# Kernel tuning notes

Hardware: AMD Instinct MI355X
Metric: run time of the kernel (lower is better)

The kernel has to match this reference:

```python
import jax, jax.numpy as jnp
import numpy as np

RESOLUTIONS = [33, 65, 129, 257, 513]
BAL = 0.5
K_CONFLICT = 3  # fixed unrolled conflict-resolution passes per level


def _up2(x):
    """Exact 2x-1 bilinear upsample with align_corners=True. [H,W]->[2H-1,2W-1]."""
    H, W = x.shape
    y = jnp.zeros((2 * H - 1, W), x.dtype)
    y = y.at[::2].set(x).at[1::2].set(0.5 * (x[:-1] + x[1:]))
    z = jnp.zeros((2 * H - 1, 2 * W - 1), x.dtype)
    z = z.at[:, ::2].set(y).at[:, 1::2].set(0.5 * (y[:, :-1] + y[:, 1:]))
    return z


def _any3x3(mask):
    """3x3 'smooth conv > 0' == any neighbor true. bool [H,W] -> bool [H,W]."""
    x = mask.astype(jnp.float32)[None, None]
    k = jnp.ones((1, 1, 3, 3), jnp.float32)
    y = jax.lax.conv_general_dilated(x, k, (1, 1), ((1, 1), (1, 1)))
    return y[0, 0] > 0


def setup_inputs() -> dict:
    key = jax.random.key(0)
    ks = jax.random.split(key, 4)
    d = 128
    return {
        "W1": jax.random.normal(ks[0], (2, d), jnp.float32) * 1.0,
        "b1": jnp.zeros((d,), jnp.float32),
        "W2": jax.random.normal(ks[1], (d, d), jnp.float32) / np.sqrt(d),
        "b2": jnp.zeros((d,), jnp.float32),
        "W3": jax.random.normal(ks[2], (d, 1), jnp.float32) * (2.0 / np.sqrt(d)),
        "b3": jnp.zeros((1,), jnp.float32),
        "b_min": jnp.zeros((2,), jnp.float32),
        "b_max": jnp.ones((2,), jnp.float32),
    }


def reference(W1, b1, W2, b2, W3, b3, b_min, b_max):
    def eval_grid(H, W):
        # align_corners=True: grid coords / (res-1) in [0,1], identical at every level
        u = jnp.linspace(0.0, 1.0, W, dtype=jnp.float32)
        v = jnp.linspace(0.0, 1.0, H, dtype=jnp.float32)
        X, Y = jnp.meshgrid(u, v)          # [H,W] each
        pts = jnp.stack([X, Y], -1).reshape(-1, 2)
        pts = b_min + pts * (b_max - b_min)
        h = jnp.tanh(pts @ W1 + b1)
        h = jnp.tanh(h @ W2 + b2)
        return jax.nn.sigmoid(h @ W3 + b3).reshape(H, W)

    Rf = RESOLUTIONS[-1]
    R0 = RESOLUTIONS[0]
    occ = eval_grid(R0, R0)                       # level-0 full evaluation
    calc = jnp.zeros((Rf, Rf), bool)
    s0 = (Rf - 1) // (R0 - 1)
    calc = calc.at[::s0, ::s0].set(True)

    for R in RESOLUTIONS[1:]:
        s = (Rf - 1) // (R - 1)
        occ_i = _up2(occ)                          # bilinear interp, align_corners=True
        valid = _up2((occ > BAL).astype(occ.dtype))
        boundary = (valid > 0) & (valid < 1)       # crossing band
        boundary = _any3x3(boundary)               # smooth_conv3x3 > 0
        calc_lvl = calc[::s, ::s]
        boundary = boundary & ~calc_lvl            # exclude already-evaluated points
        q = eval_grid(R, R)                        # query_func on level grid (masked use)
        conflicts = boundary & ((occ_i - BAL) * (q - BAL) < 0)
        occ = jnp.where(boundary, q, occ_i)        # scatter query values at boundary
        calc_lvl = calc_lvl | boundary
        # conflict resolution: re-evaluate 8-neighborhood of conflicting points
        for _ in range(K_CONFLICT):
            cand = _any3x3(conflicts) & ~calc_lvl
            conflicts = cand & ((occ - BAL) * (q - BAL) < 0)
            occ = jnp.where(cand, q, occ)
            calc_lvl = calc_lvl | cand
        calc = calc.at[::s, ::s].set(calc_lvl)

    return occ[None, None]                         # [1, 1, Rf, Rf]
```

## Files before the change

kernel.cpp:

```cpp
#include <hip/hip_runtime.h>

typedef unsigned char u8;
typedef float f32x4 __attribute__((ext_vector_type(4)));
typedef _Float16 f16x8 __attribute__((ext_vector_type(8)));

#define DIM 128
#define TM  128

__device__ __forceinline__ float fast_tanh(float x) {
    float e = __builtin_amdgcn_exp2f(x * 2.885390081777927f);
    return 1.0f - 2.0f * __builtin_amdgcn_rcpf(e + 1.0f);
}
__device__ __forceinline__ float fast_sigmoid(float x) {
    float e = __builtin_amdgcn_exp2f(x * -1.4426950408889634f);
    return __builtin_amdgcn_rcpf(1.0f + e);
}

template<int NT>
__device__ __forceinline__ void stage_w2(const float* __restrict__ W2,
                                         _Float16* sW2T, int tid) {
    #pragma unroll
    for (int s = 0; s < 2048 / NT; ++s) {
        int chunk = s * NT + tid;
        int n = chunk & 127, ko = chunk >> 7;
        f16x8 v;
        #pragma unroll
        for (int qq = 0; qq < 8; ++qq)
            v[qq] = (_Float16)W2[(ko * 8 + qq) * DIM + n];
        int slot = ko ^ (n & 15);
        *(f16x8*)&sW2T[n * DIM + slot * 8] = v;
    }
}

__device__ __forceinline__ void mlp_wave(
    const float xs[2], const float ys[2], const _Float16* sW2T,
    const float* __restrict__ W1, const float* __restrict__ b1,
    const float* __restrict__ b2, const float* __restrict__ W3,
    int lg, int l15, float rs[2][4])
{
    f32x4 acc[2][8];
    #pragma unroll
    for (int nf = 0; nf < 8; ++nf) {
        float b2v = b2[nf * 16 + l15];
        acc[0][nf] = (f32x4)(b2v);
        acc[1][nf] = (f32x4)(b2v);
    }
    #pragma unroll
    for (int kf = 0; kf < 4; ++kf) {
        const int kbase = kf * 32 + lg * 8;
        f16x8 bh[8];
        #pragma unroll
        for (int nf = 0; nf < 8; ++nf) {
            int cc = nf * 16 + l15;
            int slot = (kf * 4 + lg) ^ l15;
            bh[nf] = *(const f16x8*)&sW2T[cc * DIM + slot * 8];
        }
        f32x4 wxa = *(const f32x4*)&W1[kbase];
        f32x4 wxb = *(const f32x4*)&W1[kbase + 4];
        f32x4 wya = *(const f32x4*)&W1[DIM + kbase];
        f32x4 wyb = *(const f32x4*)&W1[DIM + kbase + 4];
        f32x4 b1a = *(const f32x4*)&b1[kbase];
        f32x4 b1b = *(const f32x4*)&b1[kbase + 4];
        f16x8 ah[2];
        #pragma unroll
        for (int mf = 0; mf < 2; ++mf) {
            float x = xs[mf], y = ys[mf];
            #pragma unroll
            for (int qq = 0; qq < 4; ++qq)
                ah[mf][qq] = (_Float16)fast_tanh(fmaf(x, wxa[qq], fmaf(y, wya[qq], b1a[qq])));
            #pragma unroll
            for (int qq = 0; qq < 4; ++qq)
                ah[mf][4 + qq] = (_Float16)fast_tanh(fmaf(x, wxb[qq], fmaf(y, wyb[qq], b1b[qq])));
        }
        #pragma unroll
        for (int nf = 0; nf < 8; ++nf)
            #pragma unroll
            for (int mf = 0; mf < 2; ++mf)
                acc[mf][nf] = __builtin_amdgcn_mfma_f32_16x16x32_f16(ah[mf], bh[nf], acc[mf][nf], 0, 0, 0);
    }
    #pragma unroll
    for (int mf = 0; mf < 2; ++mf)
        #pragma unroll
        for (int rg = 0; rg < 4; ++rg) rs[mf][rg] = 0.0f;
    #pragma unroll
    for (int nf = 0; nf < 8; ++nf) {
        float w3v = W3[nf * 16 + l15];
        #pragma unroll
        for (int mf = 0; mf < 2; ++mf)
            #pragma unroll
            for (int rg = 0; rg < 4; ++rg)
                rs[mf][rg] += fast_tanh(acc[mf][nf][rg]) * w3v;
    }
    #pragma unroll
    for (int mf = 0; mf < 2; ++mf)
        #pragma unroll
        for (int rg = 0; rg < 4; ++rg) {
            float v = rs[mf][rg];
            v += __shfl_xor(v, 1);
            v += __shfl_xor(v, 2);
            v += __shfl_xor(v, 4);
            v += __shfl_xor(v, 8);
            rs[mf][rg] = v;
        }
}

__global__ __launch_bounds__(256, 4) void eval_grid(
    const float* __restrict__ W1, const float* __restrict__ b1,
    const float* __restrict__ W2, const float* __restrict__ b2,
    const float* __restrict__ W3, const float* __restrict__ b3,
    const float* __restrict__ bmin, const float* __restrict__ bmax,
    float* __restrict__ out, int R)
{
    __shared__ __align__(16) _Float16 sW2T[DIM * DIM];
    const int N = R * R;
    const int tid = threadIdx.x;
    const int m0 = blockIdx.x * TM;
    stage_w2<256>(W2, sW2T, tid);

    const int w = tid >> 6, lane = tid & 63;
    const int l15 = lane & 15, lg = lane >> 4;

    const float inv = 1.0f / (float)(R - 1);
    const float bx0 = bmin[0], by0 = bmin[1];
    const float sx = bmax[0] - bx0, sy = bmax[1] - by0;
    float xs[2], ys[2];
    #pragma unroll
    for (int mf = 0; mf < 2; ++mf) {
        int pi = m0 + w * 32 + mf * 16 + l15;
        int pg = (pi < N) ? pi : N - 1;
        int gi = pg / R, gj = pg - gi * R;
        xs[mf] = bx0 + (float)gj * inv * sx;
        ys[mf] = by0 + (float)gi * inv * sy;
    }
    __syncthreads();

    float rs[2][4];
    mlp_wave(xs, ys, sW2T, W1, b1, b2, W3, lg, l15, rs);
    if (l15 == 0) {
        float b3v = b3[0];
        #pragma unroll
        for (int mf = 0; mf < 2; ++mf)
            #pragma unroll
            for (int rg = 0; rg < 4; ++rg) {
                int po = m0 + w * 32 + mf * 16 + lg * 4 + rg;
                if (po < N) out[po] = fast_sigmoid(rs[mf][rg] + b3v);
            }
    }
}

__global__ __launch_bounds__(512, 4) void eval_fine(
    const float* __restrict__ W1, const float* __restrict__ b1,
    const float* __restrict__ W2, const float* __restrict__ b2,
    const float* __restrict__ W3, const float* __restrict__ b3,
    const float* __restrict__ bmin, const float* __restrict__ bmax,
    const float* __restrict__ occ3, float* __restrict__ q4)
{
    __shared__ __align__(16) _Float16 sW2T[DIM * DIM];
    const int bi = blockIdx.x / 33, bj = blockIdx.x - bi * 33;
    const int ti0 = bi * 16, tj0 = bj * 16;
    const int tid = threadIdx.x;

    bool need = false;
    for (int s = tid; s < 576; s += 512) {
        int li = s / 24, lj = s - li * 24;
        int fi = ti0 - 4 + li, fj = tj0 - 4 + lj;
        if (fi >= 0 && fi < 513 && fj >= 0 && fj < 513) {
            int oi = fi & 1, oj = fj & 1;
            if (oi | oj) {
                int ip = fi >> 1, jp = fj >> 1;
                bool m0 = occ3[ip * 257 + jp] > 0.5f;
                bool b;
                if (oi && !oj)      b = m0 != (occ3[(ip + 1) * 257 + jp] > 0.5f);
                else if (!oi && oj) b = m0 != (occ3[ip * 257 + jp + 1] > 0.5f);
                else {
                    bool m1 = occ3[(ip + 1) * 257 + jp] > 0.5f;
                    bool m2 = occ3[ip * 257 + jp + 1] > 0.5f;
                    bool m3 = occ3[(ip + 1) * 257 + jp + 1] > 0.5f;
                    b = (m0 | m1 | m2 | m3) && !(m0 & m1 & m2 & m3);
                }
                need |= b;
            }
        }
    }
    if (!__syncthreads_or(need ? 1 : 0)) return;

    stage_w2<512>(W2, sW2T, tid);
    __syncthreads();

    const int w = tid >> 6, lane = tid & 63;
    const int l15 = lane & 15, lg = lane >> 4;
    const float inv = 1.0f / 512.0f;
    const float bx0 = bmin[0], by0 = bmin[1];
    const float sx = bmax[0] - bx0, sy = bmax[1] - by0;

    float xs[2], ys[2];
    #pragma unroll
    for (int mf = 0; mf < 2; ++mf) {
        int p = w * 32 + mf * 16 + l15;
        int gi = ti0 + (p >> 4), gj = tj0 + (p & 15);
        if (gi > 512) gi = 512;
        if (gj > 512) gj = 512;
        xs[mf] = bx0 + (float)gj * inv * sx;
        ys[mf] = by0 + (float)gi * inv * sy;
    }
    float rs[2][4];
    mlp_wave(xs, ys, sW2T, W1, b1, b2, W3, lg, l15, rs);
    if (l15 == 0) {
        float b3v = b3[0];
        #pragma unroll
        for (int mf = 0; mf < 2; ++mf)
            #pragma unroll
            for (int rg = 0; rg < 4; ++rg) {
                int p = w * 32 + mf * 16 + lg * 4 + rg;
                int gi = ti0 + (p >> 4), gj = tj0 + (p & 15);
                if (gi < 513 && gj < 513)
                    q4[gi * 513 + gj] = fast_sigmoid(rs[mf][rg] + b3v);
            }
    }
}

#define HWF 24
#define NTF 576
template<bool FIRST>
__device__ __forceinline__ void run_level(
    int c, int li, int lj, int oi0, int oj0, int R,
    const float* __restrict__ qbuf, int qpitch, int qs,
    const float* __restrict__ q257, int pOi, int pOj,
    const float* sOccP, const u8* sCalP,
    u8* sRaw, u8* sCfA, u8* sCfB,
    float& occR, bool& calR)
{
    const float BAL = 0.5f;
    const int fi = oi0 + li, fj = oj0 + lj;
    const bool inG = (fi >= 0 && fi < R && fj >= 0 && fj < R);
    float occ = 0.5f, qv = 0.5f;
    u8 rw = 0; bool cal = false;
    if (inG) qv = qbuf[(fi * qs) * qpitch + fj * qs];
    if (inG) {
        int ip = fi >> 1, jp = fj >> 1;
        int oi = fi & 1, oj = fj & 1;
        float tl = FIRST ? q257[(ip * 8) * 257 + jp * 8]
                         : sOccP[(ip - pOi) * HWF + (jp - pOj)];
        bool b;
        if (!oi && !oj) { occ = tl; b = false; }
        else if (oi && !oj) {
            float bl = FIRST ? q257[((ip + 1) * 8) * 257 + jp * 8]
                             : sOccP[(ip + 1 - pOi) * HWF + (jp - pOj)];
            occ = 0.5f * (tl + bl);
            b = (tl > BAL) != (bl > BAL);
        } else if (!oi && oj) {
            float tr = FIRST ? q257[(ip * 8) * 257 + (jp + 1) * 8]
                             : sOccP[(ip - pOi) * HWF + (jp + 1 - pOj)];
            occ = 0.5f * (tl + tr);
            b = (tl > BAL) != (tr > BAL);
        } else {
            float bl = FIRST ? q257[((ip + 1) * 8) * 257 + jp * 8]
                             : sOccP[(ip + 1 - pOi) * HWF + (jp - pOj)];
            float tr = FIRST ? q257[(ip * 8) * 257 + (jp + 1) * 8]
                             : sOccP[(ip - pOi) * HWF + (jp + 1 - pOj)];
            float br = FIRST ? q257[((ip + 1) * 8) * 257 + (jp + 1) * 8]
                             : sOccP[(ip + 1 - pOi) * HWF + (jp + 1 - pOj)];
            occ = 0.5f * (0.5f * (tl + bl) + 0.5f * (tr + br));
            bool m0 = tl > BAL, m1 = bl > BAL, m2 = tr > BAL, m3 = br > BAL;
            b = (m0 | m1 | m2 | m3) && !(m0 & m1 & m2 & m3);
        }
        rw = b ? 1 : 0;
        if (((fi | fj) & 1) == 0)
            cal = FIRST ? true : (sCalP[(ip - pOi) * HWF + (jp - pOj)] != 0);
    }
    sRaw[c] = rw; sCfA[c] = 0; sCfB[c] = 0;

    if (__syncthreads_or(rw)) {
        u8 cf = 0;
        if (li >= 1 && li < HWF - 1 && lj >= 1 && lj < HWF - 1 && inG) {
            bool b = false;
            #pragma unroll
            for (int di = -1; di <= 1; ++di)
                #pragma unroll
                for (int dj = -1; dj <= 1; ++dj)
                    if (sRaw[(li + di) * HWF + (lj + dj)]) b = true;
            b = b && !cal;
            cf = (b && (occ - BAL) * (qv - BAL) < 0.0f) ? 1 : 0;
            if (b) { occ = qv; cal = true; }
            sCfA[c] = cf;
        }
        int haveCf = __syncthreads_or((int)cf);

        #pragma unroll
        for (int it = 0; it < 3; ++it) {
            if (!haveCf) break;
            const u8* cin = (it & 1) ? sCfB : sCfA;
            u8* cout      = (it & 1) ? sCfA : sCfB;
            int lo = 2 + it, hi = HWF - 2 - it;
            u8 nc = 0;
            if (li >= lo && li < hi && lj >= lo && lj < hi && inG) {
                bool any = false;
                #pragma unroll
                for (int di = -1; di <= 1; ++di)
                    #pragma unroll
                    for (int dj = -1; dj <= 1; ++dj)
                        if (cin[(li + di) * HWF + (lj + dj)]) any = true;
                bool cand = any && !cal;
                nc = (cand && (occ - BAL) * (qv - BAL) < 0.0f) ? 1 : 0;
                if (cand) { occ = qv; cal = true; }
                cout[c] = nc;
            }
            haveCf = __syncthreads_or((int)nc);
        }
    }
    occR = occ; calR = cal;
}

__global__ __launch_bounds__(NTF) void levels123_fused(
    const float* __restrict__ q257,
    float* __restrict__ occ257, u8* __restrict__ cal257)
{
    __shared__ float sOcc[NTF];
    __shared__ u8 sCal[NTF], sRaw[NTF], sCfA[NTF], sCfB[NTF];
    const int bi = blockIdx.x / 17, bj = blockIdx.x - bi * 17;
    const int c = threadIdx.x;
    const int li = c / HWF, lj = c - li * HWF;
    float occ; bool cal;

    run_level<true>(c, li, lj, 4 * bi - 7, 4 * bj - 7, 65,
                    q257, 257, 4, q257, 0, 0,
                    sOcc, sCal, sRaw, sCfA, sCfB, occ, cal);
    sOcc[c] = occ; sCal[c] = cal ? 1 : 0;
    __syncthreads();
    run_level<false>(c, li, lj, 8 * bi - 6, 8 * bj - 6, 129,
                     q257, 257, 2, q257, 4 * bi - 7, 4 * bj - 7,
                     sOcc, sCal, sRaw, sCfA, sCfB, occ, cal);
    sOcc[c] = occ; sCal[c] = cal ? 1 : 0;
    __syncthreads();
    run_level<false>(c, li, lj, 16 * bi - 4, 16 * bj - 4, 257,
                     q257, 257, 1, q257, 8 * bi - 6, 8 * bj - 6,
                     sOcc, sCal, sRaw, sCfA, sCfB, occ, cal);

    const int fi = 16 * bi - 4 + li, fj = 16 * bj - 4 + lj;
    if (li >= 4 && li < 20 && lj >= 4 && lj < 20 && fi < 257 && fj < 257) {
        occ257[fi * 257 + fj] = occ;
        cal257[fi * 257 + fj] = cal ? 1 : 0;
    }
}

__global__ __launch_bounds__(NTF) void level4_kernel(
    const float* __restrict__ occP, const u8* __restrict__ calcP,
    const float* __restrict__ q4, float* __restrict__ out)
{
    __shared__ u8 sRaw[NTF], sCfA[NTF], sCfB[NTF];
    const int bi = blockIdx.x / 33, bj = blockIdx.x - bi * 33;
    const int fi0 = bi * 16 - 4, fj0 = bj * 16 - 4;
    const int c = threadIdx.x;
    const int li = c / HWF, lj = c - li * HWF;
    const int fi = fi0 + li, fj = fj0 + lj;
    const bool inG = (fi >= 0 && fi < 513 && fj >= 0 && fj < 513);
    const float BAL = 0.5f;

    float occ = 0.5f, qv = 0.5f;
    u8 rw = 0; bool cal = false;
    if (inG) qv = q4[fi * 513 + fj];
    if (inG) {
        int ip = fi >> 1, jp = fj >> 1;
        float tl = occP[ip * 257 + jp];
        int oi = fi & 1, oj = fj & 1;
        bool b;
        if (!oi && !oj) { occ = tl; b = false; }
        else if (oi && !oj) {
            float bl = occP[(ip + 1) * 257 + jp];
            occ = 0.5f * (tl + bl);
            b = (tl > BAL) != (bl > BAL);
        } else if (!oi && oj) {
            float tr = occP[ip * 257 + jp + 1];
            occ = 0.5f * (tl + tr);
            b = (tl > BAL) != (tr > BAL);
        } else {
            float bl = occP[(ip + 1) * 257 + jp];
            float tr = occP[ip * 257 + jp + 1];
            float br = occP[(ip + 1) * 257 + jp + 1];
            occ = 0.5f * (0.5f * (tl + bl) + 0.5f * (tr + br));
            bool m0 = tl > BAL, m1 = bl > BAL, m2 = tr > BAL, m3 = br > BAL;
            b = (m0 | m1 | m2 | m3) && !(m0 & m1 & m2 & m3);
        }
        rw = b ? 1 : 0;
        if (((fi | fj) & 1) == 0) cal = calcP[ip * 257 + jp] != 0;
    }
    sRaw[c] = rw; sCfA[c] = 0; sCfB[c] = 0;

    if (__syncthreads_or(rw)) {
        u8 cf = 0;
        if (li >= 1 && li < HWF - 1 && lj >= 1 && lj < HWF - 1 && inG) {
            bool b = false;
            #pragma unroll
            for (int di = -1; di <= 1; ++di)
                #pragma unroll
                for (int dj = -1; dj <= 1; ++dj)
                    if (sRaw[(li + di) * HWF + (lj + dj)]) b = true;
            b = b && !cal;
            cf = (b && (occ - BAL) * (qv - BAL) < 0.0f) ? 1 : 0;
            if (b) { occ = qv; cal = true; }
            sCfA[c] = cf;
        }
        int haveCf = __syncthreads_or((int)cf);

        #pragma unroll
        for (int it = 0; it < 3; ++it) {
            if (!haveCf) break;
            const u8* cin = (it & 1) ? sCfB : sCfA;
            u8* cout      = (it & 1) ? sCfA : sCfB;
            int lo = 2 + it, hi = HWF - 2 - it;
            u8 nc = 0;
            if (li >= lo && li < hi && lj >= lo && lj < hi && inG) {
                bool any = false;
                #pragma unroll
                for (int di = -1; di <= 1; ++di)
                    #pragma unroll
                    for (int dj = -1; dj <= 1; ++dj)
                        if (cin[(li + di) * HWF + (lj + dj)]) any = true;
                bool cand = any && !cal;
                nc = (cand && (occ - BAL) * (qv - BAL) < 0.0f) ? 1 : 0;
                if (cand) { occ = qv; cal = true; }
                cout[c] = nc;
            }
            haveCf = __syncthreads_or((int)nc);
        }
    }

    if (li >= 4 && li < 20 && lj >= 4 && lj < 20 && inG)
        out[fi * 513 + fj] = occ;
}

extern "C" void kernel_launch(void* const* d_in, const int* in_sizes, int n_in,
                              void* d_out, int out_size, void* d_ws, size_t ws_size,
                              hipStream_t stream) {
    const float* W1   = (const float*)d_in[0];
    const float* b1   = (const float*)d_in[1];
    const float* W2   = (const float*)d_in[2];
    const float* b2   = (const float*)d_in[3];
    const float* W3   = (const float*)d_in[4];
    const float* b3   = (const float*)d_in[5];
    const float* bmin = (const float*)d_in[6];
    const float* bmax = (const float*)d_in[7];

    const int N513 = 513 * 513, N257 = 257 * 257;
    float* q257   = (float*)d_ws;
    float* occ257 = q257 + N257;
    float* q4     = occ257 + N257;
    u8*    cal257 = (u8*)(q4 + N513);
    float* out    = (float*)d_out;

    eval_grid<<<(N257 + TM - 1) / TM, 256, 0, stream>>>(
        W1, b1, W2, b2, W3, b3, bmin, bmax, q257, 257);

    levels123_fused<<<17 * 17, NTF, 0, stream>>>(q257, occ257, cal257);

    eval_fine<<<33 * 33, 512, 0, stream>>>(
        W1, b1, W2, b2, W3, b3, bmin, bmax, occ257, q4);

    level4_kernel<<<33 * 33, NTF, 0, stream>>>(occ257, cal257, q4, out);
}
```

Measured before the change: 45.93 us.

## Fuse fine-level MLP evaluation into level-4 refinement kernel

Removes the separate eval_fine kernel and the q4 global buffer, evaluating the MLP directly inside the level-4 kernel for all 576 halo cells of each 24x24 tile and keeping results in shared memory. This saves a kernel launch and a global write/read round trip of the fine query grid. The cost is recomputing the 4-cell halo overlap (576 vs 256 cells per tile, over twice the MLP work for active tiles), fewer waves per MLP pass at 576 threads, and higher shared memory use per block, which lowers occupancy.

```diff
diff --git a/kernel.cpp b/kernel.cpp
--- a/kernel.cpp
+++ b/kernel.cpp
@@ -16,12 +16,9 @@
     return __builtin_amdgcn_rcpf(1.0f + e);
 }
 
-template<int NT>
 __device__ __forceinline__ void stage_w2(const float* __restrict__ W2,
-                                         _Float16* sW2T, int tid) {
-    #pragma unroll
-    for (int s = 0; s < 2048 / NT; ++s) {
-        int chunk = s * NT + tid;
+                                         _Float16* sW2T, int tid, int nt) {
+    for (int chunk = tid; chunk < 2048; chunk += nt) {
         int n = chunk & 127, ko = chunk >> 7;
         f16x8 v;
         #pragma unroll
@@ -115,7 +112,7 @@
     const int N = R * R;
     const int tid = threadIdx.x;
     const int m0 = blockIdx.x * TM;
-    stage_w2<256>(W2, sW2T, tid);
+    stage_w2(W2, sW2T, tid, 256);
 
     const int w = tid >> 6, lane = tid & 63;
     const int l15 = lane & 15, lg = lane >> 4;
@@ -144,77 +141,6 @@
             for (int rg = 0; rg < 4; ++rg) {
                 int po = m0 + w * 32 + mf * 16 + lg * 4 + rg;
                 if (po < N) out[po] = fast_sigmoid(rs[mf][rg] + b3v);
-            }
-    }
-}
-
-__global__ __launch_bounds__(512, 4) void eval_fine(
-    const float* __restrict__ W1, const float* __restrict__ b1,
-    const float* __restrict__ W2, const float* __restrict__ b2,
-    const float* __restrict__ W3, const float* __restrict__ b3,
-    const float* __restrict__ bmin, const float* __restrict__ bmax,
-    const float* __restrict__ occ3, float* __restrict__ q4)
-{
-    __shared__ __align__(16) _Float16 sW2T[DIM * DIM];
-    const int bi = blockIdx.x / 33, bj = blockIdx.x - bi * 33;
-    const int ti0 = bi * 16, tj0 = bj * 16;
-    const int tid = threadIdx.x;
-
-    bool need = false;
-    for (int s = tid; s < 576; s += 512) {
-        int li = s / 24, lj = s - li * 24;
-        int fi = ti0 - 4 + li, fj = tj0 - 4 + lj;
-        if (fi >= 0 && fi < 513 && fj >= 0 && fj < 513) {
-            int oi = fi & 1, oj = fj & 1;
-            if (oi | oj) {
-                int ip = fi >> 1, jp = fj >> 1;
-                bool m0 = occ3[ip * 257 + jp] > 0.5f;
-                bool b;
-                if (oi && !oj)      b = m0 != (occ3[(ip + 1) * 257 + jp] > 0.5f);
-                else if (!oi && oj) b = m0 != (occ3[ip * 257 + jp + 1] > 0.5f);
-                else {
-                    bool m1 = occ3[(ip + 1) * 257 + jp] > 0.5f;
-                    bool m2 = occ3[ip * 257 + jp + 1] > 0.5f;
-                    bool m3 = occ3[(ip + 1) * 257 + jp + 1] > 0.5f;
-                    b = (m0 | m1 | m2 | m3) && !(m0 & m1 & m2 & m3);
-                }
-                need |= b;
-            }
-        }
-    }
-    if (!__syncthreads_or(need ? 1 : 0)) return;
-
-    stage_w2<512>(W2, sW2T, tid);
-    __syncthreads();
-
-    const int w = tid >> 6, lane = tid & 63;
-    const int l15 = lane & 15, lg = lane >> 4;
-    const float inv = 1.0f / 512.0f;
-    const float bx0 = bmin[0], by0 = bmin[1];
-    const float sx = bmax[0] - bx0, sy = bmax[1] - by0;
-
-    float xs[2], ys[2];
-    #pragma unroll
-    for (int mf = 0; mf < 2; ++mf) {
-        int p = w * 32 + mf * 16 + l15;
-        int gi = ti0 + (p >> 4), gj = tj0 + (p & 15);
-        if (gi > 512) gi = 512;
-        if (gj > 512) gj = 512;
-        xs[mf] = bx0 + (float)gj * inv * sx;
-        ys[mf] = by0 + (float)gi * inv * sy;
-    }
-    float rs[2][4];
-    mlp_wave(xs, ys, sW2T, W1, b1, b2, W3, lg, l15, rs);
-    if (l15 == 0) {
-        float b3v = b3[0];
-        #pragma unroll
-        for (int mf = 0; mf < 2; ++mf)
-            #pragma unroll
-            for (int rg = 0; rg < 4; ++rg) {
-                int p = w * 32 + mf * 16 + lg * 4 + rg;
-                int gi = ti0 + (p >> 4), gj = tj0 + (p & 15);
-                if (gi < 513 && gj < 513)
-                    q4[gi * 513 + gj] = fast_sigmoid(rs[mf][rg] + b3v);
             }
     }
 }
@@ -343,22 +269,28 @@
     }
 }
 
-__global__ __launch_bounds__(NTF) void level4_kernel(
+__global__ __launch_bounds__(NTF) void level4_fused(
+    const float* __restrict__ W1, const float* __restrict__ b1,
+    const float* __restrict__ W2, const float* __restrict__ b2,
+    const float* __restrict__ W3, const float* __restrict__ b3,
+    const float* __restrict__ bmin, const float* __restrict__ bmax,
     const float* __restrict__ occP, const u8* __restrict__ calcP,
-    const float* __restrict__ q4, float* __restrict__ out)
+    float* __restrict__ out)
 {
+    __shared__ __align__(16) _Float16 sW2T[DIM * DIM];
+    __shared__ float sQ[NTF];
     __shared__ u8 sRaw[NTF], sCfA[NTF], sCfB[NTF];
     const int bi = blockIdx.x / 33, bj = blockIdx.x - bi * 33;
     const int fi0 = bi * 16 - 4, fj0 = bj * 16 - 4;
-    const int c = threadIdx.x;
+    const int tid = threadIdx.x;
+    const int c = tid;
     const int li = c / HWF, lj = c - li * HWF;
     const int fi = fi0 + li, fj = fj0 + lj;
     const bool inG = (fi >= 0 && fi < 513 && fj >= 0 && fj < 513);
     const float BAL = 0.5f;
 
-    float occ = 0.5f, qv = 0.5f;
+    float occ = 0.5f;
     u8 rw = 0; bool cal = false;
-    if (inG) qv = q4[fi * 513 + fj];
     if (inG) {
         int ip = fi >> 1, jp = fj >> 1;
         float tl = occP[ip * 257 + jp];
@@ -386,7 +318,72 @@
     }
     sRaw[c] = rw; sCfA[c] = 0; sCfB[c] = 0;
 
-    if (__syncthreads_or(rw)) {
+    if (!__syncthreads_or(rw)) {
+        if (li >= 4 && li < 20 && lj >= 4 && lj < 20 && inG)
+            out[fi * 513 + fj] = occ;
+        return;
+    }
+
+    stage_w2(W2, sW2T, tid, NTF);
+    __syncthreads();
+
+    const int w = tid >> 6, lane = tid & 63;
+    const int l15 = lane & 15, lg = lane >> 4;
+    const float inv = 1.0f / 512.0f;
+    const float bx0 = bmin[0], by0 = bmin[1];
+    const float sx = bmax[0] - bx0, sy = bmax[1] - by0;
+    const float b3v = b3[0];
+
+    {
+        float xs[2], ys[2];
+        #pragma unroll
+        for (int mf = 0; mf < 2; ++mf) {
+            int cell = w * 32 + mf * 16 + l15;
+            int gi = fi0 + cell / 24, gj = fj0 + cell % 24;
+            gi = gi < 0 ? 0 : (gi > 512 ? 512 : gi);
+            gj = gj < 0 ? 0 : (gj > 512 ? 512 : gj);
+            xs[mf] = bx0 + (float)gj * inv * sx;
+            ys[mf] = by0 + (float)gi * inv * sy;
+        }
+        float rs[2][4];
+        mlp_wave(xs, ys, sW2T, W1, b1, b2, W3, lg, l15, rs);
+        if (l15 == 0) {
+            #pragma unroll
+            for (int mf = 0; mf < 2; ++mf)
+                #pragma unroll
+                for (int rg = 0; rg < 4; ++rg) {
+                    int cell = w * 32 + mf * 16 + lg * 4 + rg;
+                    sQ[cell] = fast_sigmoid(rs[mf][rg] + b3v);
+                }
+        }
+    }
+    {
+        float xs[2], ys[2];
+        #pragma unroll
+        for (int mf = 0; mf < 2; ++mf) {
+            int cell = 288 + w * 32 + mf * 16 + l15;
+            int gi = fi0 + cell / 24, gj = fj0 + cell % 24;
+            gi = gi < 0 ? 0 : (gi > 512 ? 512 : gi);
+            gj = gj < 0 ? 0 : (gj > 512 ? 512 : gj);
+            xs[mf] = bx0 + (float)gj * inv * sx;
+            ys[mf] = by0 + (float)gi * inv * sy;
+        }
+        float rs[2][4];
+        mlp_wave(xs, ys, sW2T, W1, b1, b2, W3, lg, l15, rs);
+        if (l15 == 0) {
+            #pragma unroll
+            for (int mf = 0; mf < 2; ++mf)
+                #pragma unroll
+                for (int rg = 0; rg < 4; ++rg) {
+                    int cell = 288 + w * 32 + mf * 16 + lg * 4 + rg;
+                    sQ[cell] = fast_sigmoid(rs[mf][rg] + b3v);
+                }
+        }
+    }
+    __syncthreads();
+    const float qv = sQ[c];
+
+    {
         u8 cf = 0;
         if (li >= 1 && li < HWF - 1 && lj >= 1 && lj < HWF - 1 && inG) {
             bool b = false;
@@ -441,11 +438,10 @@
     const float* bmin = (const float*)d_in[6];
     const float* bmax = (const float*)d_in[7];
 
-    const int N513 = 513 * 513, N257 = 257 * 257;
+    const int N257 = 257 * 257;
     float* q257   = (float*)d_ws;
     float* occ257 = q257 + N257;
-    float* q4     = occ257 + N257;
-    u8*    cal257 = (u8*)(q4 + N513);
+    u8*    cal257 = (u8*)(occ257 + N257);
     float* out    = (float*)d_out;
 
     eval_grid<<<(N257 + TM - 1) / TM, 256, 0, stream>>>(
@@ -453,8 +449,6 @@
 
     levels123_fused<<<17 * 17, NTF, 0, stream>>>(q257, occ257, cal257);
 
-    eval_fine<<<33 * 33, 512, 0, stream>>>(
-        W1, b1, W2, b2, W3, b3, bmin, bmax, occ257, q4);
-
-    level4_kernel<<<33 * 33, NTF, 0, stream>>>(occ257, cal257, q4, out);
-}
+    level4_fused<<<33 * 33, NTF, 0, stream>>>(
+        W1, b1, W2, b2, W3, b3, bmin, bmax, occ257, cal257, out);
+}
```

Result: slower. 88.06 us (+91.7%).
